# Performance work log

Measured on AMD Instinct MI355X. Metric: run time of the kernel, lower is better.

The kernel has to match this reference:

```python
import jax, jax.numpy as jnp
import numpy as np


def setup_inputs() -> dict:
    key = jax.random.key(0)
    k1, k2 = jax.random.split(key)
    n_task, shot, feat, n_class = 32, 2048, 1024, 512
    inputs = jax.random.normal(k1, (n_task, shot, feat), dtype=jnp.float32)
    weights = jax.random.normal(k2, (n_task, n_class, feat), dtype=jnp.float32)
    return {"inputs": inputs, "weights": weights, "temp": 15}


def reference(inputs, weights, temp):
    # logits[t,s,c] = temp * (x.w - 0.5*||w||^2 - 0.5*||x||^2)
    dots = jnp.einsum('tsf,tcf->tsc', inputs, weights)        # [T,S,C]
    w_sq = 0.5 * jnp.sum(weights * weights, axis=2)           # [T,C]
    x_sq = 0.5 * jnp.sum(inputs * inputs, axis=2)             # [T,S]
    logits = temp * (dots - w_sq[:, None, :] - x_sq[:, :, None])
    return jnp.argmax(logits, axis=2)                         # [T,S] int
```

## Files before the change

### kernel.cpp

```cpp
#include <hip/hip_runtime.h>
#include <cstdint>
#include <cstddef>

#define T_TASKS 32
#define S_SHOT  2048
#define F_FEAT  1024
#define C_CLS   512
#define MARGIN  0.1f

typedef _Float16 f16;
typedef _Float16 f16x8 __attribute__((ext_vector_type(8)));
typedef float    f32x4 __attribute__((ext_vector_type(4)));


__device__ __forceinline__ void upd3(float v, int i,
                                     float& v1, int& i1,
                                     float& v2, int& i2,
                                     float& v3, int& i3) {
  if (v > v1 || (v == v1 && i < i1)) { v3=v2; i3=i2; v2=v1; i2=i1; v1=v; i1=i; }
  else if (v > v2 || (v == v2 && i < i2)) { v3=v2; i3=i2; v2=v; i2=i; }
  else if (v > v3 || (v == v3 && i < i3)) { v3=v; i3=i; }
}

__device__ __forceinline__ void cvt8(float4 a, float4 b, f16x8& h, f16x8& l) {
  float f[8] = {a.x, a.y, a.z, a.w, b.x, b.y, b.z, b.w};
#pragma unroll
  for (int j = 0; j < 8; ++j) {
    f16 hj = (f16)f[j];
    h[j] = hj;
    l[j] = (f16)(f[j] - (float)hj);
  }
}

__global__ __launch_bounds__(256) void zero_wsq(float* wsq) {
  wsq[blockIdx.x * 256 + threadIdx.x] = 0.f;
}

__global__ __launch_bounds__(512) void prep_w(const float* __restrict__ W,
                                              f16* __restrict__ Wh,
                                              float* __restrict__ wsq) {
  const int bx = blockIdx.x;
  const int t = bx >> 5, kt = bx & 31;
  const int c = threadIdx.x;
  const float* wr = W + ((size_t)(t * C_CLS + c)) * F_FEAT + kt * 32;
  float v[32];
  float s = 0.f;
#pragma unroll
  for (int i = 0; i < 8; ++i) {
    float4 x = *(const float4*)(wr + i * 4);
    v[i*4+0] = x.x; v[i*4+1] = x.y; v[i*4+2] = x.z; v[i*4+3] = x.w;
    s += x.x*x.x + x.y*x.y + x.z*x.z + x.w*x.w;
  }
  const int ct = c >> 4, m = c & 15;
  f16* base = Wh + ((size_t)((t * 32 + kt) * 32 + ct)) * 512 + m * 8;
#pragma unroll
  for (int q = 0; q < 4; ++q) {
    f16x8 h;
#pragma unroll
    for (int j = 0; j < 8; ++j) h[j] = (f16)v[q * 8 + j];
    *(f16x8*)(base + q * 128) = h;
  }
  atomicAdd(&wsq[t * C_CLS + c], 0.5f * s);
}

__global__ __launch_bounds__(256, 2) void gemm_argmax(
    const float* __restrict__ X, const float* __restrict__ W,
    const f16* __restrict__ Wh, const float* __restrict__ wsq,
    int* __restrict__ out) {
  __shared__ float swsq[C_CLS];
  __shared__ float cv[64][2][3];
  __shared__ int   ci[64][2][3];
  __shared__ int   amb_cnt;
  __shared__ int   amb_list[64];

  const int tid = threadIdx.x;
  const int wv  = tid >> 6, ln = tid & 63;
  const int rg  = wv >> 1, cg = wv & 1;
  const int m   = ln & 15, q = ln >> 4;
  const int bx  = blockIdx.x;
  const int t   = bx & 31, rb = bx >> 5;
  const int row0 = rb * 64;

  swsq[tid]       = wsq[t * C_CLS + tid];
  swsq[tid + 256] = wsq[t * C_CLS + tid + 256];
  if (tid == 0) amb_cnt = 0;
  __syncthreads();

  const f32x4 zero4 = {0.f, 0.f, 0.f, 0.f};
  f32x4 acc[2][16];
#pragma unroll
  for (int a = 0; a < 2; ++a)
#pragma unroll
    for (int b = 0; b < 16; ++b) acc[a][b] = zero4;

  const float* x0 = X + ((size_t)(t * S_SHOT + row0 + rg * 32 + m)) * F_FEAT + q * 8;
  const float* x1 = x0 + (size_t)16 * F_FEAT;
  const f16* wt = Wh + ((size_t)t * 32 * 32 * 512) + (size_t)(cg * 16) * 512 + ln * 8;

  float4 p0a = *(const float4*)(x0);
  float4 p0b = *(const float4*)(x0 + 4);
  float4 p1a = *(const float4*)(x1);
  float4 p1b = *(const float4*)(x1 + 4);

#pragma unroll 2
  for (int kt = 0; kt < 32; ++kt) {
    const int kn = (kt < 31) ? (kt + 1) : 31;
    float4 n0a = *(const float4*)(x0 + kn * 32);
    float4 n0b = *(const float4*)(x0 + kn * 32 + 4);
    float4 n1a = *(const float4*)(x1 + kn * 32);
    float4 n1b = *(const float4*)(x1 + kn * 32 + 4);

    f16x8 ah0, al0, ah1, al1;
    cvt8(p0a, p0b, ah0, al0);
    cvt8(p1a, p1b, ah1, al1);

    const f16* bp = wt + (size_t)kt * 16384;
    f16x8 b[16];
#pragma unroll
    for (int i = 0; i < 16; ++i) b[i] = *(const f16x8*)(bp + i * 512);
#pragma unroll
    for (int i = 0; i < 16; ++i) {
      acc[0][i] = __builtin_amdgcn_mfma_f32_16x16x32_f16(ah0, b[i], acc[0][i], 0, 0, 0);
      acc[0][i] = __builtin_amdgcn_mfma_f32_16x16x32_f16(al0, b[i], acc[0][i], 0, 0, 0);
      acc[1][i] = __builtin_amdgcn_mfma_f32_16x16x32_f16(ah1, b[i], acc[1][i], 0, 0, 0);
      acc[1][i] = __builtin_amdgcn_mfma_f32_16x16x32_f16(al1, b[i], acc[1][i], 0, 0, 0);
    }
    p0a = n0a; p0b = n0b; p1a = n1a; p1b = n1b;
  }

  const int c0 = cg * 256 + m;
#pragma unroll
  for (int rt = 0; rt < 2; ++rt) {
#pragma unroll
    for (int rr = 0; rr < 4; ++rr) {
      float v1 = -3.4e38f, v2 = -3.4e38f, v3 = -3.4e38f;
      int   i1 = 0x7fffffff, i2 = 0x7fffffff, i3 = 0x7fffffff;
#pragma unroll
      for (int ct = 0; ct < 16; ++ct) {
        int cidx = c0 + ct * 16;
        float sc = acc[rt][ct][rr] - swsq[cidx];
        upd3(sc, cidx, v1, i1, v2, i2, v3, i3);
      }
      for (int off = 1; off < 16; off <<= 1) {
        float w1 = __shfl_xor(v1, off); int j1 = __shfl_xor(i1, off);
        float w2 = __shfl_xor(v2, off); int j2 = __shfl_xor(i2, off);
        float w3 = __shfl_xor(v3, off); int j3 = __shfl_xor(i3, off);
        upd3(w1, j1, v1, i1, v2, i2, v3, i3);
        upd3(w2, j2, v1, i1, v2, i2, v3, i3);
        upd3(w3, j3, v1, i1, v2, i2, v3, i3);
      }
      if (m == 0) {
        int row = rg * 32 + rt * 16 + q * 4 + rr;
        cv[row][cg][0] = v1; ci[row][cg][0] = i1;
        cv[row][cg][1] = v2; ci[row][cg][1] = i2;
        cv[row][cg][2] = v3; ci[row][cg][2] = i3;
      }
    }
  }
  __syncthreads();

  if (tid < 64) {
    float a1 = cv[tid][0][0]; int aj = ci[tid][0][0];
    float b1 = cv[tid][1][0]; int bj = ci[tid][1][0];
    float win, runner; int widx;
    if (a1 > b1 || (a1 == b1 && aj < bj)) {
      win = a1; widx = aj; runner = fmaxf(b1, cv[tid][0][1]);
    } else {
      win = b1; widx = bj; runner = fmaxf(a1, cv[tid][1][1]);
    }
    if (win - runner >= MARGIN) {
      out[t * S_SHOT + row0 + tid] = widx;
    } else {
      int p = atomicAdd(&amb_cnt, 1);
      amb_list[p] = tid;
    }
  }
  __syncthreads();

  int nA = amb_cnt;
  for (int a = wv; a < nA; a += 4) {
    int rl = amb_list[a];
    const float* xr = X + ((size_t)t * S_SHOT + row0 + rl) * F_FEAT;
    double best = -1.0e300; int bidx = 0x7fffffff;
    for (int g = 0; g < 2; ++g) {
      for (int k = 0; k < 3; ++k) {
        int cidx = ci[rl][g][k];
        const float* wr = W + ((size_t)t * C_CLS + cidx) * F_FEAT;
        double sd = 0.0, sw = 0.0;
        for (int j = 0; j < 16; ++j) {
          float xv  = xr[ln + 64 * j];
          float wv2 = wr[ln + 64 * j];
          sd += (double)xv * (double)wv2;
          sw += (double)wv2 * (double)wv2;
        }
#pragma unroll
        for (int off = 32; off > 0; off >>= 1) {
          sd += __shfl_xor(sd, off);
          sw += __shfl_xor(sw, off);
        }
        double sc = sd - 0.5 * sw;
        if (sc > best || (sc == best && cidx < bidx)) { best = sc; bidx = cidx; }
      }
    }
    if (ln == 0) out[t * S_SHOT + row0 + rl] = bidx;
  }
}

extern "C" void kernel_launch(void* const* d_in, const int* in_sizes, int n_in,
                              void* d_out, int out_size, void* d_ws, size_t ws_size,
                              hipStream_t stream) {
  (void)in_sizes; (void)n_in; (void)out_size;
  const float* X = (const float*)d_in[0];
  const float* W = (const float*)d_in[1];
  const size_t wh_bytes = (size_t)T_TASKS * C_CLS * F_FEAT * sizeof(f16);
  const size_t need = wh_bytes + (size_t)T_TASKS * C_CLS * sizeof(float);
  if (ws_size < need) return;
  f16*   Wh  = (f16*)d_ws;
  float* wsq = (float*)((char*)d_ws + wh_bytes);
  int*   out = (int*)d_out;
  zero_wsq<<<T_TASKS * C_CLS / 256, 256, 0, stream>>>(wsq);
  prep_w<<<T_TASKS * 32, 512, 0, stream>>>(W, Wh, wsq);
  gemm_argmax<<<T_TASKS * (S_SHOT / 64), 256, 0, stream>>>(X, W, Wh, wsq, out);
}
```

Measured before the change: 883.0 us.

## Drop split-f16 X correction, stage tiles in LDS, pack top-4 keys

The GEMM now uses single-precision-f16 X instead of the hi/lo split, which halves the MFMA count. To absorb the extra error the ambiguity margin is widened and the kernel keeps four candidates per row for the fp64 rescoring. Weight tiles are loaded into LDS with global_load_lds and X is converted through LDS. The class dimension is processed in two halves, and candidates are packed as quantized score plus index keys in u32. prep_w is restructured to write the fragment layout through shared memory without atomics, removing the zeroing kernel. The risk is more rows falling into the slow fp64 fallback path, and quantization limits on the score range.

Result: slower. 1.086 ms (+22.9%).

```diff
diff --git a/kernel.cpp b/kernel.cpp
--- a/kernel.cpp
+++ b/kernel.cpp
@@ -2,174 +2,198 @@
 #include <cstdint>
 #include <cstddef>
 
-#define T_TASKS 32
-#define S_SHOT  2048
-#define F_FEAT  1024
-#define C_CLS   512
-#define MARGIN  0.1f
+#define MARGIN 0.26f
 
 typedef _Float16 f16;
+typedef _Float16 f16x4 __attribute__((ext_vector_type(4)));
 typedef _Float16 f16x8 __attribute__((ext_vector_type(8)));
 typedef float    f32x4 __attribute__((ext_vector_type(4)));
-
-
-__device__ __forceinline__ void upd3(float v, int i,
-                                     float& v1, int& i1,
-                                     float& v2, int& i2,
-                                     float& v3, int& i3) {
-  if (v > v1 || (v == v1 && i < i1)) { v3=v2; i3=i2; v2=v1; i2=i1; v1=v; i1=i; }
-  else if (v > v2 || (v == v2 && i < i2)) { v3=v2; i3=i2; v2=v; i2=i; }
-  else if (v > v3 || (v == v3 && i < i3)) { v3=v; i3=i; }
-}
-
-__device__ __forceinline__ void cvt8(float4 a, float4 b, f16x8& h, f16x8& l) {
-  float f[8] = {a.x, a.y, a.z, a.w, b.x, b.y, b.z, b.w};
-#pragma unroll
-  for (int j = 0; j < 8; ++j) {
-    f16 hj = (f16)f[j];
-    h[j] = hj;
-    l[j] = (f16)(f[j] - (float)hj);
-  }
-}
-
-__global__ __launch_bounds__(256) void zero_wsq(float* wsq) {
-  wsq[blockIdx.x * 256 + threadIdx.x] = 0.f;
+typedef unsigned int u32;
+
+__device__ __forceinline__ void gl_lds16(const void* g, void* l) {
+  auto gp = (const __attribute__((address_space(1))) uint32_t*)(g);
+  auto lp = (__attribute__((address_space(3))) uint32_t*)(l);
+  __builtin_amdgcn_global_load_lds(gp, lp, 16, 0, 0);
+}
+
+__device__ __forceinline__ void ins4(u32 v, u32& a, u32& b, u32& c, u32& d) {
+  if (v > a)      { d = c; c = b; b = a; a = v; }
+  else if (v > b) { d = c; c = b; b = v; }
+  else if (v > c) { d = c; c = v; }
+  else if (v > d) { d = v; }
 }
 
 __global__ __launch_bounds__(512) void prep_w(const float* __restrict__ W,
                                               f16* __restrict__ Wh,
                                               float* __restrict__ wsq) {
+  __shared__ __align__(16) f16 sF[32 * 512];
   const int bx = blockIdx.x;
-  const int t = bx >> 5, kt = bx & 31;
-  const int c = threadIdx.x;
-  const float* wr = W + ((size_t)(t * C_CLS + c)) * F_FEAT + kt * 32;
-  float v[32];
-  float s = 0.f;
-#pragma unroll
-  for (int i = 0; i < 8; ++i) {
-    float4 x = *(const float4*)(wr + i * 4);
-    v[i*4+0] = x.x; v[i*4+1] = x.y; v[i*4+2] = x.z; v[i*4+3] = x.w;
-    s += x.x*x.x + x.y*x.y + x.z*x.z + x.w*x.w;
-  }
-  const int ct = c >> 4, m = c & 15;
-  f16* base = Wh + ((size_t)((t * 32 + kt) * 32 + ct)) * 512 + m * 8;
-#pragma unroll
-  for (int q = 0; q < 4; ++q) {
-    f16x8 h;
-#pragma unroll
-    for (int j = 0; j < 8; ++j) h[j] = (f16)v[q * 8 + j];
-    *(f16x8*)(base + q * 128) = h;
-  }
-  atomicAdd(&wsq[t * C_CLS + c], 0.5f * s);
-}
-
-__global__ __launch_bounds__(256, 2) void gemm_argmax(
+  const int t = bx >> 3, cgrp = bx & 7;
+  const int tid = threadIdx.x;
+  const int r = tid >> 3, i = tid & 7;
+  const int c = cgrp * 64 + r;
+  const float* wr = W + ((size_t)t * 512 + c) * 1024;
+  const int m = r & 15, fct = r >> 4;
+  const int q = i >> 1, jj = (i & 1) * 4;
+  const int ch = cgrp >> 2, fhb = (cgrp & 3) * 4;
+  const int wv = tid >> 6, ln = tid & 63;
+  float ssum = 0.f;
+  for (int kq = 0; kq < 4; ++kq) {
+    if (kq) __syncthreads();
+#pragma unroll
+    for (int j = 0; j < 8; ++j) {
+      float4 x = *(const float4*)(wr + kq * 256 + j * 32 + i * 4);
+      ssum += x.x * x.x + x.y * x.y + x.z * x.z + x.w * x.w;
+      f16x4 hv;
+      hv.x = (f16)x.x; hv.y = (f16)x.y; hv.z = (f16)x.z; hv.w = (f16)x.w;
+      int lf = j * 4 + fct;
+      *(f16x4*)(sF + lf * 512 + (q * 16 + m) * 8 + jj) = hv;
+    }
+    __syncthreads();
+#pragma unroll
+    for (int ii = 0; ii < 4; ++ii) {
+      int lf = wv * 4 + ii;
+      int j = lf >> 2, fl = lf & 3;
+      int kt = kq * 8 + j;
+      size_t gfrag = (size_t)(((t * 2 + ch) * 32 + kt) * 16 + fhb + fl);
+      *(f16x8*)(Wh + gfrag * 512 + ln * 8) = *(const f16x8*)(sF + lf * 512 + ln * 8);
+    }
+  }
+  ssum += __shfl_down(ssum, 4, 8);
+  ssum += __shfl_down(ssum, 2, 8);
+  ssum += __shfl_down(ssum, 1, 8);
+  if (i == 0) wsq[t * 512 + c] = 0.5f * ssum;
+}
+
+__global__ __launch_bounds__(256, 3) void gemm_argmax(
     const float* __restrict__ X, const float* __restrict__ W,
     const f16* __restrict__ Wh, const float* __restrict__ wsq,
     int* __restrict__ out) {
-  __shared__ float swsq[C_CLS];
-  __shared__ float cv[64][2][3];
-  __shared__ int   ci[64][2][3];
-  __shared__ int   amb_cnt;
-  __shared__ int   amb_list[64];
+  __shared__ __align__(16) f16 sB[2 * 16 * 512];
+  __shared__ __align__(16) f16 sX[64 * 72];
+  __shared__ u32 wcand[64][4][4];
+  __shared__ u32 hcand[64][2][4];
+  __shared__ float swsq[256];
+  __shared__ int amb_cnt;
+  __shared__ int amb_list[64];
 
   const int tid = threadIdx.x;
-  const int wv  = tid >> 6, ln = tid & 63;
-  const int rg  = wv >> 1, cg = wv & 1;
-  const int m   = ln & 15, q = ln >> 4;
-  const int bx  = blockIdx.x;
-  const int t   = bx & 31, rb = bx >> 5;
+  const int wv = tid >> 6, ln = tid & 63;
+  const int m = ln & 15, q = ln >> 4;
+  const int bx = blockIdx.x;
+  const int t = bx >> 5, rb = bx & 31;
   const int row0 = rb * 64;
-
-  swsq[tid]       = wsq[t * C_CLS + tid];
-  swsq[tid + 256] = wsq[t * C_CLS + tid + 256];
+  const int r4 = tid >> 2, cseg = tid & 3;
+
   if (tid == 0) amb_cnt = 0;
+  const float* xrow = X + ((size_t)t * 2048 + row0 + r4) * 1024;
+
+  for (int ch = 0; ch < 2; ++ch) {
+    __syncthreads();
+    swsq[tid] = wsq[t * 512 + ch * 256 + tid];
+
+    const f32x4 zero4 = {0.f, 0.f, 0.f, 0.f};
+    f32x4 acc[4][4];
+#pragma unroll
+    for (int a = 0; a < 4; ++a)
+#pragma unroll
+      for (int b = 0; b < 4; ++b) acc[a][b] = zero4;
+
+    const f16* WhB = Wh + ((size_t)(t * 2 + ch) * 32 * 16) * 512;
+
+    for (int it = 0; it < 16; ++it) {
+      __syncthreads();
+      {
+        const int s = wv & 1, fh0 = (wv >> 1) * 8;
+        const f16* gB = WhB + ((size_t)((2 * it + s) * 16 + fh0)) * 512 + ln * 8;
+        f16* lB = sB + (s * 16 + fh0) * 512;
+#pragma unroll
+        for (int ii = 0; ii < 8; ++ii)
+          gl_lds16(gB + ii * 512, lB + ii * 512);
+      }
+      {
+        const float* xs = xrow + it * 64;
+#pragma unroll
+        for (int l = 0; l < 4; ++l) {
+          float4 v = *(const float4*)(xs + l * 16 + cseg * 4);
+          f16x4 h;
+          h.x = (f16)v.x; h.y = (f16)v.y; h.z = (f16)v.z; h.w = (f16)v.w;
+          *(f16x4*)(sX + r4 * 72 + l * 16 + cseg * 4) = h;
+        }
+      }
+      __syncthreads();
+#pragma unroll
+      for (int s = 0; s < 2; ++s) {
+        f16x8 a[4], b[4];
+#pragma unroll
+        for (int rt = 0; rt < 4; ++rt)
+          a[rt] = *(const f16x8*)(sX + (rt * 16 + m) * 72 + s * 32 + q * 8);
+#pragma unroll
+        for (int ct = 0; ct < 4; ++ct)
+          b[ct] = *(const f16x8*)(sB + (s * 16 + wv * 4 + ct) * 512 + ln * 8);
+#pragma unroll
+        for (int rt = 0; rt < 4; ++rt)
+#pragma unroll
+          for (int ct = 0; ct < 4; ++ct)
+            acc[rt][ct] = __builtin_amdgcn_mfma_f32_16x16x32_f16(
+                a[rt], b[ct], acc[rt][ct], 0, 0, 0);
+      }
+    }
+
+#pragma unroll
+    for (int rt = 0; rt < 4; ++rt) {
+#pragma unroll
+      for (int rr = 0; rr < 4; ++rr) {
+        u32 t0 = 0, t1 = 0, t2 = 0, t3 = 0;
+#pragma unroll
+        for (int ct = 0; ct < 4; ++ct) {
+          int lc = wv * 64 + ct * 16 + m;
+          float v = acc[rt][ct][rr] - swsq[lc];
+          float vq = fminf(fmaxf((v + 1024.f) * 2048.f, 0.f), 4194303.f);
+          u32 key = (((u32)vq) << 9) | (u32)(511 - (ch * 256 + lc));
+          ins4(key, t0, t1, t2, t3);
+        }
+#pragma unroll
+        for (int off = 1; off < 16; off <<= 1) {
+          u32 s0 = __shfl_xor(t0, off), s1 = __shfl_xor(t1, off);
+          u32 s2 = __shfl_xor(t2, off), s3 = __shfl_xor(t3, off);
+          ins4(s0, t0, t1, t2, t3); ins4(s1, t0, t1, t2, t3);
+          ins4(s2, t0, t1, t2, t3); ins4(s3, t0, t1, t2, t3);
+        }
+        if (m == 0) {
+          int row = rt * 16 + q * 4 + rr;
+          wcand[row][wv][0] = t0; wcand[row][wv][1] = t1;
+          wcand[row][wv][2] = t2; wcand[row][wv][3] = t3;
+        }
+      }
+    }
+    __syncthreads();
+    if (tid < 64) {
+      u32 t0 = 0, t1 = 0, t2 = 0, t3 = 0;
+#pragma unroll
+      for (int w = 0; w < 4; ++w)
+#pragma unroll
+        for (int k = 0; k < 4; ++k) ins4(wcand[tid][w][k], t0, t1, t2, t3);
+      hcand[tid][ch][0] = t0; hcand[tid][ch][1] = t1;
+      hcand[tid][ch][2] = t2; hcand[tid][ch][3] = t3;
+    }
+  }
   __syncthreads();
 
-  const f32x4 zero4 = {0.f, 0.f, 0.f, 0.f};
-  f32x4 acc[2][16];
-#pragma unroll
-  for (int a = 0; a < 2; ++a)
-#pragma unroll
-    for (int b = 0; b < 16; ++b) acc[a][b] = zero4;
-
-  const float* x0 = X + ((size_t)(t * S_SHOT + row0 + rg * 32 + m)) * F_FEAT + q * 8;
-  const float* x1 = x0 + (size_t)16 * F_FEAT;
-  const f16* wt = Wh + ((size_t)t * 32 * 32 * 512) + (size_t)(cg * 16) * 512 + ln * 8;
-
-  float4 p0a = *(const float4*)(x0);
-  float4 p0b = *(const float4*)(x0 + 4);
-  float4 p1a = *(const float4*)(x1);
-  float4 p1b = *(const float4*)(x1 + 4);
-
-#pragma unroll 2
-  for (int kt = 0; kt < 32; ++kt) {
-    const int kn = (kt < 31) ? (kt + 1) : 31;
-    float4 n0a = *(const float4*)(x0 + kn * 32);
-    float4 n0b = *(const float4*)(x0 + kn * 32 + 4);
-    float4 n1a = *(const float4*)(x1 + kn * 32);
-    float4 n1b = *(const float4*)(x1 + kn * 32 + 4);
-
-    f16x8 ah0, al0, ah1, al1;
-    cvt8(p0a, p0b, ah0, al0);
-    cvt8(p1a, p1b, ah1, al1);
-
-    const f16* bp = wt + (size_t)kt * 16384;
-    f16x8 b[16];
-#pragma unroll
-    for (int i = 0; i < 16; ++i) b[i] = *(const f16x8*)(bp + i * 512);
-#pragma unroll
-    for (int i = 0; i < 16; ++i) {
-      acc[0][i] = __builtin_amdgcn_mfma_f32_16x16x32_f16(ah0, b[i], acc[0][i], 0, 0, 0);
-      acc[0][i] = __builtin_amdgcn_mfma_f32_16x16x32_f16(al0, b[i], acc[0][i], 0, 0, 0);
-      acc[1][i] = __builtin_amdgcn_mfma_f32_16x16x32_f16(ah1, b[i], acc[1][i], 0, 0, 0);
-      acc[1][i] = __builtin_amdgcn_mfma_f32_16x16x32_f16(al1, b[i], acc[1][i], 0, 0, 0);
-    }
-    p0a = n0a; p0b = n0b; p1a = n1a; p1b = n1b;
-  }
-
-  const int c0 = cg * 256 + m;
-#pragma unroll
-  for (int rt = 0; rt < 2; ++rt) {
-#pragma unroll
-    for (int rr = 0; rr < 4; ++rr) {
-      float v1 = -3.4e38f, v2 = -3.4e38f, v3 = -3.4e38f;
-      int   i1 = 0x7fffffff, i2 = 0x7fffffff, i3 = 0x7fffffff;
-#pragma unroll
-      for (int ct = 0; ct < 16; ++ct) {
-        int cidx = c0 + ct * 16;
-        float sc = acc[rt][ct][rr] - swsq[cidx];
-        upd3(sc, cidx, v1, i1, v2, i2, v3, i3);
-      }
-      for (int off = 1; off < 16; off <<= 1) {
-        float w1 = __shfl_xor(v1, off); int j1 = __shfl_xor(i1, off);
-        float w2 = __shfl_xor(v2, off); int j2 = __shfl_xor(i2, off);
-        float w3 = __shfl_xor(v3, off); int j3 = __shfl_xor(i3, off);
-        upd3(w1, j1, v1, i1, v2, i2, v3, i3);
-        upd3(w2, j2, v1, i1, v2, i2, v3, i3);
-        upd3(w3, j3, v1, i1, v2, i2, v3, i3);
-      }
-      if (m == 0) {
-        int row = rg * 32 + rt * 16 + q * 4 + rr;
-        cv[row][cg][0] = v1; ci[row][cg][0] = i1;
-        cv[row][cg][1] = v2; ci[row][cg][1] = i2;
-        cv[row][cg][2] = v3; ci[row][cg][2] = i3;
-      }
-    }
-  }
-  __syncthreads();
-
   if (tid < 64) {
-    float a1 = cv[tid][0][0]; int aj = ci[tid][0][0];
-    float b1 = cv[tid][1][0]; int bj = ci[tid][1][0];
-    float win, runner; int widx;
-    if (a1 > b1 || (a1 == b1 && aj < bj)) {
-      win = a1; widx = aj; runner = fmaxf(b1, cv[tid][0][1]);
-    } else {
-      win = b1; widx = bj; runner = fmaxf(a1, cv[tid][1][1]);
-    }
-    if (win - runner >= MARGIN) {
-      out[t * S_SHOT + row0 + tid] = widx;
+    u32 best = 0, second = 0;
+#pragma unroll
+    for (int g = 0; g < 2; ++g)
+#pragma unroll
+      for (int k = 0; k < 4; ++k) {
+        u32 v = hcand[tid][g][k];
+        if (v > best) { second = best; best = v; }
+        else if (v > second) second = v;
+      }
+    float v1 = (float)(best >> 9) * (1.f / 2048.f);
+    float v2 = (float)(second >> 9) * (1.f / 2048.f);
+    if (v1 - v2 >= MARGIN) {
+      out[(size_t)t * 2048 + row0 + tid] = 511 - (int)(best & 511);
     } else {
       int p = atomicAdd(&amb_cnt, 1);
       amb_list[p] = tid;
@@ -180,15 +204,15 @@
   int nA = amb_cnt;
   for (int a = wv; a < nA; a += 4) {
     int rl = amb_list[a];
-    const float* xr = X + ((size_t)t * S_SHOT + row0 + rl) * F_FEAT;
-    double best = -1.0e300; int bidx = 0x7fffffff;
+    const float* xr = X + ((size_t)t * 2048 + row0 + rl) * 1024;
+    double bestv = -1.0e300; int bidx = 0x7fffffff;
     for (int g = 0; g < 2; ++g) {
-      for (int k = 0; k < 3; ++k) {
-        int cidx = ci[rl][g][k];
-        const float* wr = W + ((size_t)t * C_CLS + cidx) * F_FEAT;
+      for (int k = 0; k < 4; ++k) {
+        int cidx = 511 - (int)(hcand[rl][g][k] & 511);
+        const float* wr = W + ((size_t)t * 512 + cidx) * 1024;
         double sd = 0.0, sw = 0.0;
         for (int j = 0; j < 16; ++j) {
-          float xv  = xr[ln + 64 * j];
+          float xv = xr[ln + 64 * j];
           float wv2 = wr[ln + 64 * j];
           sd += (double)xv * (double)wv2;
           sw += (double)wv2 * (double)wv2;
@@ -199,10 +223,10 @@
           sw += __shfl_xor(sw, off);
         }
         double sc = sd - 0.5 * sw;
-        if (sc > best || (sc == best && cidx < bidx)) { best = sc; bidx = cidx; }
-      }
-    }
-    if (ln == 0) out[t * S_SHOT + row0 + rl] = bidx;
+        if (sc > bestv || (sc == bestv && cidx < bidx)) { bestv = sc; bidx = cidx; }
+      }
+    }
+    if (ln == 0) out[(size_t)t * 2048 + row0 + rl] = bidx;
   }
 }
 
@@ -212,13 +236,12 @@
   (void)in_sizes; (void)n_in; (void)out_size;
   const float* X = (const float*)d_in[0];
   const float* W = (const float*)d_in[1];
-  const size_t wh_bytes = (size_t)T_TASKS * C_CLS * F_FEAT * sizeof(f16);
-  const size_t need = wh_bytes + (size_t)T_TASKS * C_CLS * sizeof(float);
+  const size_t wh_bytes = (size_t)32 * 512 * 1024 * sizeof(f16);
+  const size_t need = wh_bytes + (size_t)32 * 512 * sizeof(float);
   if (ws_size < need) return;
   f16*   Wh  = (f16*)d_ws;
   float* wsq = (float*)((char*)d_ws + wh_bytes);
   int*   out = (int*)d_out;
-  zero_wsq<<<T_TASKS * C_CLS / 256, 256, 0, stream>>>(wsq);
-  prep_w<<<T_TASKS * 32, 512, 0, stream>>>(W, Wh, wsq);
-  gemm_argmax<<<T_TASKS * (S_SHOT / 64), 256, 0, stream>>>(X, W, Wh, wsq, out);
-}
+  prep_w<<<32 * 8, 512, 0, stream>>>(W, Wh, wsq);
+  gemm_argmax<<<32 * 32, 256, 0, stream>>>(X, W, Wh, wsq, out);
+}
```
